# Performance work log

Hardware: AMD Instinct MI355X
Metric: run time of the kernel (lower is better)

The kernel has to match this reference:

```python
import jax, jax.numpy as jnp
import numpy as np
import math

IN_C, OUT_C, KH, KW = 128, 128, 3, 3
GROUPS_NUM, NUM_W = 8, 8
STRIDE, PAD, DIL = 1, 1, 1
BETA = 1.0


def setup_inputs() -> dict:
    key = jax.random.key(0)
    ks = jax.random.split(key, 6)
    B, H, W = 8, 56, 56
    n = IN_C * KH * KW
    bound = math.sqrt(6.0 / n)  # reset_parameters bound for weight templates
    inputs = jax.random.normal(ks[0], (B, IN_C, H, W), jnp.float32)
    mask = jax.random.randint(ks[1], (B, H, W), 0, GROUPS_NUM)
    Alpha = jax.random.uniform(ks[2], (B, GROUPS_NUM, H, W), jnp.float32)
    weight_templates = jax.random.uniform(ks[3], (OUT_C * IN_C * KH * KW, NUM_W), jnp.float32, -bound, bound)
    routing_w = jax.random.normal(ks[4], (GROUPS_NUM * NUM_W, IN_C), jnp.float32) * 0.01
    routing_b = jnp.zeros((GROUPS_NUM * NUM_W,), jnp.float32)
    bias = jnp.zeros((OUT_C,), jnp.float32)
    return dict(inputs=inputs, mask=mask, Alpha=Alpha, weight_templates=weight_templates,
                routing_w=routing_w, routing_b=routing_b, bias=bias, use_alpha=1)


def _unfold(x):
    # torch F.unfold-compatible im2col: [B, C*KH*KW, Ho, Wo], channel-major feature order
    return jax.lax.conv_general_dilated_patches(
        x, (KH, KW), (STRIDE, STRIDE), [(PAD, PAD), (PAD, PAD)],
        rhs_dilation=(DIL, DIL), dimension_numbers=('NCHW', 'OIHW', 'NCHW'))


def reference(inputs, mask, Alpha, weight_templates, routing_w, routing_b, bias, use_alpha):
    B, C, H, W = inputs.shape
    K = IN_C * KH * KW
    # SE-style routing: GAP -> fc -> scaled sigmoid (alpha=1.0 in source)
    x_se = inputs.reshape(B, C, -1).mean(-1)                              # [B, C]
    x_se = 2.0 * jax.nn.sigmoid(x_se @ routing_w.T + routing_b) / NUM_W   # [B, G*num_W]
    # blend weight templates: F.linear(x_se.reshape(-1,num_W), weight)
    w = x_se.reshape(B * GROUPS_NUM, NUM_W) @ weight_templates.T          # [B*G, O*K]
    w = w.reshape(B, GROUPS_NUM, OUT_C, K).transpose(0, 2, 3, 1)          # [B, O, K, G]
    patches = _unfold(inputs)                                             # [B, K, Ho, Wo]
    # per-group convolution outputs, then per-pixel group routing
    y = jnp.einsum('bokg,bkhw->boghw', w, patches)                        # [B, O, G, Ho, Wo]
    if use_alpha:
        probs = jax.nn.softmax(BETA * Alpha, axis=1)                      # soft routing [B, G, Ho, Wo]
    else:
        probs = jax.nn.one_hot(mask, GROUPS_NUM, axis=1, dtype=y.dtype)   # hard per-pixel group select
    out = jnp.einsum('boghw,bghw->bohw', y, probs)
    return out + bias.reshape(1, -1, 1, 1)
```

## Files before the change

### kernel.cpp

```cpp
#include <hip/hip_runtime.h>
#include <stdint.h>

#define IN_C   128
#define OUT_C  128
#define KTOT   1152
#define NG     8
#define NW     8
#define NB     8
#define HH     56
#define WWID   56
#define NPIX   3136
#define MTOT   1024
#define HALO   58
#define HPIX   (HALO*HALO)


typedef __attribute__((ext_vector_type(8))) short short8;
typedef __attribute__((ext_vector_type(8))) unsigned short ushort8;
typedef __attribute__((ext_vector_type(4))) float f32x4;

__device__ __forceinline__ unsigned short f2bf(float f) {
    unsigned u = __float_as_uint(f);
    u += 0x7FFF + ((u >> 16) & 1);
    return (unsigned short)(u >> 16);
}

__device__ __forceinline__ void cp16(const unsigned short* g, unsigned short* l) {
    __builtin_amdgcn_global_load_lds(
        (const __attribute__((address_space(1))) unsigned int*)g,
        (__attribute__((address_space(3))) unsigned int*)l,
        16, 0, 0);
}

__global__ __launch_bounds__(256) void prep_kernel(const float* __restrict__ in,
                                                   const float* __restrict__ T,
                                                   float* __restrict__ xse,
                                                   unsigned short* __restrict__ Apack,
                                                   unsigned short* __restrict__ Xt) {
    __shared__ __align__(16) unsigned char smem[36864];
    const int blk = blockIdx.x;
    const int t = threadIdx.x;

    if (blk < 1024) {
        const float* src = in + (size_t)blk * NPIX;
        float s = 0.f;
        for (int i = t; i < NPIX / 4; i += 256) {
            float4 v = ((const float4*)src)[i];
            s += v.x + v.y + v.z + v.w;
        }
        #pragma unroll
        for (int off = 32; off; off >>= 1) s += __shfl_down(s, off);
        float* ws4 = (float*)smem;
        if ((t & 63) == 0) ws4[t >> 6] = s;
        __syncthreads();
        if (t == 0)
            xse[blk] = (ws4[0] + ws4[1] + ws4[2] + ws4[3]) * (1.0f / (float)NPIX);
        return;
    }
    if (blk < 1152) {
        float* lf = (float*)smem;
        const int o = blk - 1024;
        const float* To = T + (size_t)o * 9216;
        #pragma unroll
        for (int it = 0; it < 9; it++) {
            const int f = it * 256 + t;
            const float4 v = ((const float4*)To)[f];
            *(float4*)&lf[f * 4] = v;
        }
        __syncthreads();
        const int m16b = o >> 1;
        const int lrb = (o & 1) * 8;
        #pragma unroll
        for (int it = 0; it < 5; it++) {
            const int ch = it * 256 + t;
            if (ch < 1152) {
                const int j = ch & 7, kc = ch >> 3;
                const int s = kc >> 4, c0 = (kc & 15) << 3;
                const int kt = kc >> 2, lq = kc & 3;
                ushort8 v;
                #pragma unroll
                for (int i = 0; i < 8; i++)
                    v[i] = f2bf(lf[((c0 + i) * 9 + s) * 8 + j]);
                const size_t off = ((((size_t)m16b * 36 + kt) * 4 + lq) * 16 + lrb + j) * 8;
                *(ushort8*)&Apack[off] = v;
            }
        }
        return;
    }
    unsigned short* tile = (unsigned short*)smem;
    const int idx = blk - 1152;
    const int yt = idx % 28;
    const int b  = idx / 28;
    const int y0 = yt * 2;

    #pragma unroll
    for (int it = 0; it < 14; it++) {
        const int f = it * 256 + t;
        const int c = f / 28;
        const int rem = f - c * 28;
        const int y = rem / 14;
        const int x4 = rem - y * 14;
        const float4 v = *(const float4*)(in + ((size_t)(b * IN_C + c)) * NPIX
                                          + (y0 + y) * WWID + x4 * 4);
        unsigned short bf0 = f2bf(v.x), bf1 = f2bf(v.y), bf2 = f2bf(v.z), bf3 = f2bf(v.w);
        const int ppb = (y * WWID + x4 * 4) ^ (((c >> 3) & 15) << 2);
        uint2 pk;
        pk.x = (unsigned)bf0 | ((unsigned)bf1 << 16);
        pk.y = (unsigned)bf2 | ((unsigned)bf3 << 16);
        *(uint2*)&tile[c * 128 + ppb] = pk;
    }
    __syncthreads();

    #pragma unroll
    for (int it = 0; it < 7; it++) {
        const int ch = it * 256 + t;
        const int oct = ch & 15;
        const int pp = ch >> 4;
        const int sw = oct << 2;
        ushort8 v;
        #pragma unroll
        for (int i = 0; i < 8; i++)
            v[i] = tile[(oct * 8 + i) * 128 + (pp ^ sw)];
        const int y2 = (pp >= WWID) ? 1 : 0;
        const int xg = pp - y2 * WWID;
        const size_t hp = (size_t)b * HPIX + (y0 + y2 + 1) * HALO + (xg + 1);
        *(ushort8*)&Xt[hp * 128 + oct * 8] = v;
    }

    if (t < 64) {
        const int pi = t >> 4, oct = t & 15;
        const int yy = y0 + 1 + (pi >> 1);
        const int xx = (pi & 1) * 57;
        *(ushort8*)&Xt[((size_t)b * HPIX + yy * HALO + xx) * 128 + oct * 8] =
            (ushort8){0, 0, 0, 0, 0, 0, 0, 0};
    }
    if (yt == 0 || yt == 27) {
        const int yy = (yt == 0) ? 0 : 57;
        #pragma unroll
        for (int it = 0; it < 4; it++) {
            const int ch = it * 256 + t;
            if (ch < 928) {
                const int xx = ch >> 4, oct = ch & 15;
                *(ushort8*)&Xt[((size_t)b * HPIX + yy * HALO + xx) * 128 + oct * 8] =
                    (ushort8){0, 0, 0, 0, 0, 0, 0, 0};
            }
        }
    }
}

__global__ __launch_bounds__(256) void gemm_kernel(const unsigned short* __restrict__ Apack,
                                                   const unsigned short* __restrict__ Xt,
                                                   const float* __restrict__ xse,
                                                   const float* __restrict__ rw,
                                                   const float* __restrict__ rb,
                                                   const float* __restrict__ Alpha,
                                                   const int* __restrict__ mask,
                                                   const int* __restrict__ use_alpha,
                                                   const float* __restrict__ bias,
                                                   float* __restrict__ out) {
    __shared__ __align__(16) unsigned short Bsh[2][1024 * 8];
    __shared__ float ssh[128 * 8];
    __shared__ float xs[IN_C];
    __shared__ float rsh[64];

    const int tid = threadIdx.x;
    const int wv = tid >> 6, ln = tid & 63;
    const int lq = ln >> 4, lr = ln & 15;
    const int wrow = wv >> 1, wcol = wv & 1;

    const int lid = blockIdx.x;
    const int b   = lid & 7;
    const int sl  = lid >> 3;
    const int mt  = sl & 7;
    const int nt  = sl >> 3;

    const unsigned short* gbp[4];
    #pragma unroll
    for (int i = 0; i < 4; i++) {
        const int r = i * 32 + (tid >> 3);
        const int q = (tid & 7) ^ (r & 3) ^ ((r >> 2) & 3);
        const int p = min(nt * 128 + r, NPIX - 1);
        const int py = p / WWID, px = p - py * WWID;
        gbp[i] = Xt + ((size_t)b * HPIX + py * HALO + px) * 128 + q * 8;
    }

    const unsigned short* gaw[4];
    #pragma unroll
    for (int tm = 0; tm < 4; tm++) {
        const int m16 = mt * 8 + wrow * 4 + tm;
        gaw[tm] = Apack + ((size_t)m16 * 36 * 64 + ln) * 8;
    }

    if (tid < IN_C) xs[tid] = xse[b * IN_C + tid];
    __syncthreads();
    if (tid < 64) {
        float acc = rb[tid];
        #pragma unroll 8
        for (int c = 0; c < IN_C; c++) acc += xs[c] * rw[tid * IN_C + c];
        rsh[tid] = 0.25f / (1.0f + expf(-acc));
    }
    __syncthreads();

    #pragma unroll
    for (int i = 0; i < 4; i++) cp16(gbp[i], &Bsh[0][(i * 256 + wv * 64) * 8]);
    short8 afA[4], afB[4];
    #pragma unroll
    for (int tm = 0; tm < 4; tm++) afA[tm] = *(const short8*)(gaw[tm]);

    if (tid < 128) {
        const int p = nt * 128 + tid;
        float sj[8] = {0, 0, 0, 0, 0, 0, 0, 0};
        if (p < NPIX) {
            if (use_alpha[0]) {
                float a[8], m = -1e30f;
                #pragma unroll
                for (int g = 0; g < 8; g++) {
                    a[g] = Alpha[((size_t)(b * NG + g)) * NPIX + p];
                    m = fmaxf(m, a[g]);
                }
                float pr[8], sum = 0.f;
                #pragma unroll
                for (int g = 0; g < 8; g++) { pr[g] = expf(a[g] - m); sum += pr[g]; }
                const float inv = 1.f / sum;
                #pragma unroll
                for (int g = 0; g < 8; g++) {
                    const float w = pr[g] * inv;
                    #pragma unroll
                    for (int j = 0; j < 8; j++) sj[j] += w * rsh[g * 8 + j];
                }
            } else {
                const int mg = mask[(size_t)b * NPIX + p];
                #pragma unroll
                for (int j = 0; j < 8; j++) sj[j] = rsh[mg * 8 + j];
            }
        }
        #pragma unroll
        for (int j = 0; j < 8; j++) ssh[tid * 8 + j] = sj[j];
    }

    f32x4 acc[4][4];
    #pragma unroll
    for (int i = 0; i < 4; i++)
        #pragma unroll
        for (int j = 0; j < 4; j++) acc[i][j] = (f32x4){0.f, 0.f, 0.f, 0.f};

    const int jx = lq ^ (lr & 3) ^ ((lr >> 2) & 3);

    #pragma unroll
    for (int st = 0; st < 18; st++) {
        const int kk = st * 64;
        const int bufc = st & 1;
        __syncthreads();
        if (st + 1 < 18) {
            const int nk = kk + 64;
            const int s  = nk >> 7;
            const int kh = s / 3, kw = s - 3 * kh;
            const int offB = (kh * HALO + kw) * 128 + (nk & 127);
            #pragma unroll
            for (int i = 0; i < 4; i++)
                cp16(gbp[i] + offB, &Bsh[bufc ^ 1][(i * 256 + wv * 64) * 8]);
        }
        #pragma unroll
        for (int tm = 0; tm < 4; tm++)
            afB[tm] = *(const short8*)(gaw[tm] + (size_t)((kk + 32) >> 5) * 512);
        {
            short8 bfr[4];
            #pragma unroll
            for (int tn = 0; tn < 4; tn++) {
                const int row = wcol * 64 + tn * 16 + lr;
                bfr[tn] = *(const short8*)&Bsh[bufc][(row * 8 + jx) * 8];
            }
            #pragma unroll
            for (int tm = 0; tm < 4; tm++)
                #pragma unroll
                for (int tn = 0; tn < 4; tn++)
                    acc[tm][tn] = __builtin_amdgcn_mfma_f32_16x16x32_bf16(
                        afA[tm], bfr[tn], acc[tm][tn], 0, 0, 0);
        }
        if (st + 1 < 18) {
            #pragma unroll
            for (int tm = 0; tm < 4; tm++)
                afA[tm] = *(const short8*)(gaw[tm] + (size_t)((kk + 64) >> 5) * 512);
        }
        {
            short8 bfr[4];
            #pragma unroll
            for (int tn = 0; tn < 4; tn++) {
                const int row = wcol * 64 + tn * 16 + lr;
                bfr[tn] = *(const short8*)&Bsh[bufc][(row * 8 + 4 + jx) * 8];
            }
            #pragma unroll
            for (int tm = 0; tm < 4; tm++)
                #pragma unroll
                for (int tn = 0; tn < 4; tn++)
                    acc[tm][tn] = __builtin_amdgcn_mfma_f32_16x16x32_bf16(
                        afB[tm], bfr[tn], acc[tm][tn], 0, 0, 0);
        }
    }

    const int j0 = (lq & 1) * 4;
    const int oo = lq >> 1;
    #pragma unroll
    for (int tm = 0; tm < 4; tm++) {
        const int o = mt * 16 + wrow * 8 + tm * 2 + oo;
        const float bo = bias[o];
        #pragma unroll
        for (int tn = 0; tn < 4; tn++) {
            const int pp = wcol * 64 + tn * 16 + lr;
            const int p = nt * 128 + pp;
            const f32x4 sv = *(const f32x4*)&ssh[pp * 8 + j0];
            const f32x4 a = acc[tm][tn];
            float part = a.x * sv.x + a.y * sv.y + a.z * sv.z + a.w * sv.w;
            float tot = part + __shfl_xor(part, 16);
            if ((lq & 1) == 0 && p < NPIX)
                out[((size_t)b * OUT_C + o) * NPIX + p] = tot + bo;
        }
    }
}

extern "C" void kernel_launch(void* const* d_in, const int* in_sizes, int n_in,
                              void* d_out, int out_size, void* d_ws, size_t ws_size,
                              hipStream_t stream) {
    const float* inputs = (const float*)d_in[0];
    const int*   mask   = (const int*)d_in[1];
    const float* Alpha  = (const float*)d_in[2];
    const float* wtmpl  = (const float*)d_in[3];
    const float* rw     = (const float*)d_in[4];
    const float* rb     = (const float*)d_in[5];
    const float* bias   = (const float*)d_in[6];
    const int*   ua     = (const int*)d_in[7];
    float* out = (float*)d_out;

    char* ws = (char*)d_ws;
    unsigned short* Xt  = (unsigned short*)ws;
    unsigned short* Apk = (unsigned short*)(ws + 6889472);
    float*          xse = (float*)(ws + 9248768);

    prep_kernel<<<1376, 256, 0, stream>>>(inputs, wtmpl, xse, Apk, Xt);
    gemm_kernel<<<1600, 256, 0, stream>>>(Apk, Xt, xse, rw, rb, Alpha, mask, ua, bias, out);
}
```

Baseline: 171.2 us.

## Halve GEMM K-step to 32 with smaller LDS buffers; convert templates to bf16 early

The GEMM main loop now stages 32 K-elements per step instead of 64. Each step loads a 512-row shared buffer, so LDS use drops, and the loop runs 36 synchronised iterations instead of 18. A-fragments are double-buffered in registers across steps. The prep kernel also converts weight templates to bf16 as it stages them into shared memory, which halves that buffer. The main risk is twice as many barriers and smaller transfers per step, which may weaken latency hiding. The gain would come from fewer LDS bytes per block, which could allow higher occupancy.

```diff
diff --git a/kernel.cpp b/kernel.cpp
--- a/kernel.cpp
+++ b/kernel.cpp
@@ -37,7 +37,7 @@
                                                    float* __restrict__ xse,
                                                    unsigned short* __restrict__ Apack,
                                                    unsigned short* __restrict__ Xt) {
-    __shared__ __align__(16) unsigned char smem[36864];
+    __shared__ __align__(16) unsigned char smem[32768];
     const int blk = blockIdx.x;
     const int t = threadIdx.x;
 
@@ -58,14 +58,16 @@
         return;
     }
     if (blk < 1152) {
-        float* lf = (float*)smem;
+        unsigned short* lh = (unsigned short*)smem;
         const int o = blk - 1024;
         const float* To = T + (size_t)o * 9216;
         #pragma unroll
         for (int it = 0; it < 9; it++) {
             const int f = it * 256 + t;
             const float4 v = ((const float4*)To)[f];
-            *(float4*)&lf[f * 4] = v;
+            ushort4 h;
+            h.x = f2bf(v.x); h.y = f2bf(v.y); h.z = f2bf(v.z); h.w = f2bf(v.w);
+            *(ushort4*)&lh[f * 4] = h;
         }
         __syncthreads();
         const int m16b = o >> 1;
@@ -80,7 +82,7 @@
                 ushort8 v;
                 #pragma unroll
                 for (int i = 0; i < 8; i++)
-                    v[i] = f2bf(lf[((c0 + i) * 9 + s) * 8 + j]);
+                    v[i] = lh[((c0 + i) * 9 + s) * 8 + j];
                 const size_t off = ((((size_t)m16b * 36 + kt) * 4 + lq) * 16 + lrb + j) * 8;
                 *(ushort8*)&Apack[off] = v;
             }
@@ -158,7 +160,7 @@
                                                    const int* __restrict__ use_alpha,
                                                    const float* __restrict__ bias,
                                                    float* __restrict__ out) {
-    __shared__ __align__(16) unsigned short Bsh[2][1024 * 8];
+    __shared__ __align__(16) unsigned short Bsh[2][512 * 8];
     __shared__ float ssh[128 * 8];
     __shared__ float xs[IN_C];
     __shared__ float rsh[64];
@@ -174,15 +176,17 @@
     const int mt  = sl & 7;
     const int nt  = sl >> 3;
 
-    const unsigned short* gbp[4];
-    #pragma unroll
-    for (int i = 0; i < 4; i++) {
-        const int r = i * 32 + (tid >> 3);
-        const int q = (tid & 7) ^ (r & 3) ^ ((r >> 2) & 3);
-        const int p = min(nt * 128 + r, NPIX - 1);
-        const int py = p / WWID, px = p - py * WWID;
-        gbp[i] = Xt + ((size_t)b * HPIX + py * HALO + px) * 128 + q * 8;
-    }
+    const int js = tid & 3;
+    const int r0 = tid >> 2,  q0 = js ^ (r0 & 3) ^ ((r0 >> 2) & 3);
+    const int r1 = r0 + 64,   q1 = js ^ (r1 & 3) ^ ((r1 >> 2) & 3);
+    const int p0 = min(nt * 128 + r0, NPIX - 1);
+    const int p1 = min(nt * 128 + r1, NPIX - 1);
+    const int y0p = p0 / WWID, x0p = p0 - y0p * WWID;
+    const int y1p = p1 / WWID, x1p = p1 - y1p * WWID;
+    const unsigned short* gb0 = Xt + ((size_t)b * HPIX + y0p * HALO + x0p) * 128 + q0 * 8;
+    const unsigned short* gb1 = Xt + ((size_t)b * HPIX + y1p * HALO + x1p) * 128 + q1 * 8;
+    unsigned short* lb0[2] = { &Bsh[0][(wv * 64) * 8],       &Bsh[1][(wv * 64) * 8] };
+    unsigned short* lb1[2] = { &Bsh[0][(256 + wv * 64) * 8], &Bsh[1][(256 + wv * 64) * 8] };
 
     const unsigned short* gaw[4];
     #pragma unroll
@@ -201,11 +205,10 @@
     }
     __syncthreads();
 
-    #pragma unroll
-    for (int i = 0; i < 4; i++) cp16(gbp[i], &Bsh[0][(i * 256 + wv * 64) * 8]);
-    short8 afA[4], afB[4];
-    #pragma unroll
-    for (int tm = 0; tm < 4; tm++) afA[tm] = *(const short8*)(gaw[tm]);
+    cp16(gb0, lb0[0]); cp16(gb1, lb1[0]);
+    short8 af[2][4];
+    #pragma unroll
+    for (int tm = 0; tm < 4; tm++) af[0][tm] = *(const short8*)(gaw[tm]);
 
     if (tid < 128) {
         const int p = nt * 128 + tid;
@@ -244,58 +247,34 @@
         #pragma unroll
         for (int j = 0; j < 4; j++) acc[i][j] = (f32x4){0.f, 0.f, 0.f, 0.f};
 
-    const int jx = lq ^ (lr & 3) ^ ((lr >> 2) & 3);
-
-    #pragma unroll
-    for (int st = 0; st < 18; st++) {
-        const int kk = st * 64;
-        const int bufc = st & 1;
+    const int jj = lq ^ (lr & 3) ^ ((lr >> 2) & 3);
+
+    #pragma unroll
+    for (int st = 0; st < 36; st++) {
+        const int buf = st & 1;
         __syncthreads();
-        if (st + 1 < 18) {
-            const int nk = kk + 64;
+        if (st + 1 < 36) {
+            const int nk = (st + 1) * 32;
             const int s  = nk >> 7;
             const int kh = s / 3, kw = s - 3 * kh;
             const int offB = (kh * HALO + kw) * 128 + (nk & 127);
-            #pragma unroll
-            for (int i = 0; i < 4; i++)
-                cp16(gbp[i] + offB, &Bsh[bufc ^ 1][(i * 256 + wv * 64) * 8]);
-        }
-        #pragma unroll
-        for (int tm = 0; tm < 4; tm++)
-            afB[tm] = *(const short8*)(gaw[tm] + (size_t)((kk + 32) >> 5) * 512);
-        {
-            short8 bfr[4];
-            #pragma unroll
-            for (int tn = 0; tn < 4; tn++) {
-                const int row = wcol * 64 + tn * 16 + lr;
-                bfr[tn] = *(const short8*)&Bsh[bufc][(row * 8 + jx) * 8];
-            }
+            cp16(gb0 + offB, lb0[buf ^ 1]); cp16(gb1 + offB, lb1[buf ^ 1]);
             #pragma unroll
             for (int tm = 0; tm < 4; tm++)
-                #pragma unroll
-                for (int tn = 0; tn < 4; tn++)
-                    acc[tm][tn] = __builtin_amdgcn_mfma_f32_16x16x32_bf16(
-                        afA[tm], bfr[tn], acc[tm][tn], 0, 0, 0);
-        }
-        if (st + 1 < 18) {
+                af[(st + 1) & 1][tm] = *(const short8*)(gaw[tm] + (size_t)(st + 1) * 512);
+        }
+        short8 bfr[4];
+        #pragma unroll
+        for (int tn = 0; tn < 4; tn++) {
+            const int row = wcol * 64 + tn * 16 + lr;
+            bfr[tn] = *(const short8*)&Bsh[buf][(row * 4 + jj) * 8];
+        }
+        #pragma unroll
+        for (int tm = 0; tm < 4; tm++)
             #pragma unroll
-            for (int tm = 0; tm < 4; tm++)
-                afA[tm] = *(const short8*)(gaw[tm] + (size_t)((kk + 64) >> 5) * 512);
-        }
-        {
-            short8 bfr[4];
-            #pragma unroll
-            for (int tn = 0; tn < 4; tn++) {
-                const int row = wcol * 64 + tn * 16 + lr;
-                bfr[tn] = *(const short8*)&Bsh[bufc][(row * 8 + 4 + jx) * 8];
-            }
-            #pragma unroll
-            for (int tm = 0; tm < 4; tm++)
-                #pragma unroll
-                for (int tn = 0; tn < 4; tn++)
-                    acc[tm][tn] = __builtin_amdgcn_mfma_f32_16x16x32_bf16(
-                        afB[tm], bfr[tn], acc[tm][tn], 0, 0, 0);
-        }
+            for (int tn = 0; tn < 4; tn++)
+                acc[tm][tn] = __builtin_amdgcn_mfma_f32_16x16x32_bf16(
+                    af[st & 1][tm], bfr[tn], acc[tm][tn], 0, 0, 0);
     }
 
     const int j0 = (lq & 1) * 4;
```

Result: no change. 171.8 us (+0.4%).
